# Performance work log

Measured on AMD Instinct MI355X. Metric: run time of the kernel, lower is better.

The kernel has to match this reference:

```python
import jax, jax.numpy as jnp
import numpy as np

N = 1536       # number of agents in the group
T = 20         # track length (only last step used)
H = 64         # hidden_size
E = 16         # embadding_size
M = 128        # PNMLP_hidden_size


def setup_inputs() -> dict:
    key = jax.random.key(0)
    ks = jax.random.split(key, 8)
    s = lambda fan_in: 1.0 / np.sqrt(fan_in)
    return {
        "hidden_state": jax.random.normal(ks[0], (N, H), dtype=jnp.float32),
        "group_track": jax.random.normal(ks[1], (N, T, 2), dtype=jnp.float32),
        "We": jax.random.uniform(ks[2], (2, E), jnp.float32, -s(2), s(2)),
        "be": jax.random.uniform(ks[3], (E,), jnp.float32, -s(2), s(2)),
        "W1": jax.random.uniform(ks[4], (E + H, M), jnp.float32, -s(E + H), s(E + H)),
        "b1": jax.random.uniform(ks[5], (M,), jnp.float32, -s(E + H), s(E + H)),
        "W2": jax.random.uniform(ks[6], (M, H), jnp.float32, -s(M), s(M)),
        "b2": jax.random.uniform(ks[7], (H,), jnp.float32, -s(M), s(M)),
    }


def reference(hidden_state, group_track, We, be, W1, b1, W2, b2):
    # end positions of every track: [N, 2]
    end = group_track[:, -1, :]
    # rel[i, j] = end[j] - end[i]  (neighbor j relative to center i): [N, N, 2]
    rel = end[None, :, :] - end[:, None, :]
    # linear embedding of relative end positions: [N, N, E]
    emb = rel @ We + be
    # concat hidden state (same for all centers) with embedding: [N, N, E+H]
    h = jnp.broadcast_to(hidden_state[None, :, :], (rel.shape[0], rel.shape[1], hidden_state.shape[1]))
    x = jnp.concatenate((h, emb), axis=-1)
    # MLP [E+H -> M -> H] with ReLU after each linear (batch_norm=False)
    x = jax.nn.relu(x @ W1 + b1)
    x = jax.nn.relu(x @ W2 + b2)
    # max-pool over neighbors j for each center i: [N, H]
    return jnp.max(x, axis=1)
```

## Files before the change

kernel.cpp:

```cpp
#include <hip/hip_runtime.h>
#include <hip/hip_fp16.h>


#define NN 1536
#define HH 64
#define EE 16
#define MM 128
#define TT 20
#define NI 2
#define IB 8
#define JSPLIT 8
#define NIGRP (NN / IB)
#define NTILE (96 / JSPLIT)

typedef _Float16 half8 __attribute__((ext_vector_type(8)));
typedef float f32x4 __attribute__((ext_vector_type(4)));

__device__ __forceinline__ void async16(const void* g, void* l) {
  __builtin_amdgcn_global_load_lds(
      (const __attribute__((address_space(1))) unsigned int*)g,
      (__attribute__((address_space(3))) unsigned int*)l, 16, 0, 0);
}

__global__ __launch_bounds__(128) void precompute_kernel(
    const float* __restrict__ hidden, const float* __restrict__ gt,
    const float* __restrict__ We, const float* __restrict__ be,
    const float* __restrict__ W1, const float* __restrict__ b1,
    const float* __restrict__ W2,
    _Float16* __restrict__ Qs, _Float16* __restrict__ P,
    _Float16* __restrict__ W2Ts, float* __restrict__ out)
{
  const int j = blockIdx.x;
  const int m = threadIdx.x;
  const float* hrow = hidden + j * HH;
  float a = 0.f;
  #pragma unroll 8
  for (int h = 0; h < HH; ++h) a = fmaf(hrow[h], W1[h * MM + m], a);
  float ve0 = 0.f, ve1 = 0.f, cm = b1[m];
  #pragma unroll
  for (int e = 0; e < EE; ++e) {
    float w1e = W1[(HH + e) * MM + m];
    ve0 = fmaf(We[e], w1e, ve0);
    ve1 = fmaf(We[EE + e], w1e, ve1);
    cm  = fmaf(be[e], w1e, cm);
  }
  const float e0 = gt[j * (2 * TT) + 2 * (TT - 1)];
  const float e1 = gt[j * (2 * TT) + 2 * (TT - 1) + 1];
  const float p = fmaf(e0, ve0, e1 * ve1);
  P[j * MM + m] = (_Float16)p;
  const int swz = ((((m >> 3) ^ (j & 15)) << 3) | (m & 7));
  Qs[j * MM + swz] = (_Float16)(a + p + cm);
  if (j < HH) W2Ts[j * MM + swz] = (_Float16)W2[m * HH + j];
  if (m < HH) out[j * HH + m] = 0.f;
}

__global__ __launch_bounds__(256) void pairmlp_max_kernel(
    const _Float16* __restrict__ Qs, const _Float16* __restrict__ P,
    const _Float16* __restrict__ W2Ts, const float* __restrict__ b2,
    float* __restrict__ out)
{
  __shared__ __align__(16) _Float16 sW[HH * MM];
  __shared__ __align__(16) _Float16 sQ[2][16 * MM];

  const int tid  = threadIdx.x;
  const int wave = tid >> 6;
  const int lane = tid & 63;
  const int quad = lane >> 4;
  const int lcol = lane & 15;
  const int ig = blockIdx.x % NIGRP;
  const int js = blockIdx.x / NIGRP;
  const int i0 = ig * IB + wave * NI;
  const int jt0 = js * NTILE;

  #pragma unroll
  for (int r = 0; r < 4; ++r)
    async16((const char*)W2Ts + tid * 16 + r * 4096, (char*)sW + tid * 16 + r * 4096);
  async16((const char*)Qs + (size_t)jt0 * 4096 + tid * 16, (char*)sQ[0] + tid * 16);

  half8 pv[NI][4];
  #pragma unroll
  for (int ii = 0; ii < NI; ++ii) {
    const _Float16* prow = P + (i0 + ii) * MM + quad * 8;
    #pragma unroll
    for (int ks = 0; ks < 4; ++ks)
      pv[ii][ks] = *(const half8*)(prow + ks * 32);
  }

  int soff[4];
  #pragma unroll
  for (int ks = 0; ks < 4; ++ks)
    soff[ks] = lcol * MM + ((((ks * 4 + quad) ^ lcol) & 15) << 3);

  float rmax[NI][4];
  #pragma unroll
  for (int ii = 0; ii < NI; ++ii)
    #pragma unroll
    for (int ct = 0; ct < 4; ++ct) rmax[ii][ct] = -1e30f;

  const half8 hz = 0;
  const f32x4 zc = {0.f, 0.f, 0.f, 0.f};

  __syncthreads();

  #pragma unroll 2
  for (int t = 0; t < NTILE; ++t) {
    const int jn = (t + 1 < NTILE) ? (jt0 + t + 1) : jt0;
    async16((const char*)Qs + (size_t)jn * 4096 + tid * 16, (char*)sQ[(t + 1) & 1] + tid * 16);

    const _Float16* qb = sQ[t & 1];
    f32x4 acc[NI][4];
    #pragma unroll
    for (int ks = 0; ks < 4; ++ks) {
      const half8 qg  = *(const half8*)(qb + soff[ks]);
      const half8 bf0 = *(const half8*)(sW + soff[ks]);
      const half8 bf1 = *(const half8*)(sW + soff[ks] + 16 * MM);
      const half8 bf2 = *(const half8*)(sW + soff[ks] + 32 * MM);
      const half8 bf3 = *(const half8*)(sW + soff[ks] + 48 * MM);
      #pragma unroll
      for (int ii = 0; ii < NI; ++ii) {
        half8 s = qg - pv[ii][ks];
        s = __builtin_elementwise_max(s, hz);
        if (ks == 0) {
          acc[ii][0] = __builtin_amdgcn_mfma_f32_16x16x32_f16(s, bf0, zc, 0, 0, 0);
          acc[ii][1] = __builtin_amdgcn_mfma_f32_16x16x32_f16(s, bf1, zc, 0, 0, 0);
          acc[ii][2] = __builtin_amdgcn_mfma_f32_16x16x32_f16(s, bf2, zc, 0, 0, 0);
          acc[ii][3] = __builtin_amdgcn_mfma_f32_16x16x32_f16(s, bf3, zc, 0, 0, 0);
        } else {
          acc[ii][0] = __builtin_amdgcn_mfma_f32_16x16x32_f16(s, bf0, acc[ii][0], 0, 0, 0);
          acc[ii][1] = __builtin_amdgcn_mfma_f32_16x16x32_f16(s, bf1, acc[ii][1], 0, 0, 0);
          acc[ii][2] = __builtin_amdgcn_mfma_f32_16x16x32_f16(s, bf2, acc[ii][2], 0, 0, 0);
          acc[ii][3] = __builtin_amdgcn_mfma_f32_16x16x32_f16(s, bf3, acc[ii][3], 0, 0, 0);
        }
      }
    }

    #pragma unroll
    for (int ii = 0; ii < NI; ++ii)
      #pragma unroll
      for (int ct = 0; ct < 4; ++ct) {
        const float m01 = fmaxf(acc[ii][ct][0], acc[ii][ct][1]);
        const float m23 = fmaxf(acc[ii][ct][2], acc[ii][ct][3]);
        rmax[ii][ct] = fmaxf(rmax[ii][ct], fmaxf(m01, m23));
      }

    __syncthreads();
  }

  #pragma unroll
  for (int ii = 0; ii < NI; ++ii)
    #pragma unroll
    for (int ct = 0; ct < 4; ++ct) {
      float v = rmax[ii][ct];
      v = fmaxf(v, __shfl_xor(v, 16, 64));
      v = fmaxf(v, __shfl_xor(v, 32, 64));
      v = fmaxf(v + b2[ct * 16 + lcol], 0.f);
      if (quad == 0)
        atomicMax((unsigned*)(out + (i0 + ii) * HH + ct * 16 + lcol), __float_as_uint(v));
    }
}

extern "C" void kernel_launch(void* const* d_in, const int* in_sizes, int n_in,
                              void* d_out, int out_size, void* d_ws, size_t ws_size,
                              hipStream_t stream) {
  const float* hidden = (const float*)d_in[0];
  const float* gt     = (const float*)d_in[1];
  const float* We     = (const float*)d_in[2];
  const float* be     = (const float*)d_in[3];
  const float* W1     = (const float*)d_in[4];
  const float* b1     = (const float*)d_in[5];
  const float* W2     = (const float*)d_in[6];
  const float* b2     = (const float*)d_in[7];
  float* out = (float*)d_out;

  _Float16* Qs   = (_Float16*)d_ws;
  _Float16* Ph   = Qs + NN * MM;
  _Float16* W2Ts = Ph + NN * MM;

  precompute_kernel<<<NN, 128, 0, stream>>>(hidden, gt, We, be, W1, b1, W2, Qs, Ph, W2Ts, out);
  pairmlp_max_kernel<<<NIGRP * JSPLIT, 256, 0, stream>>>(Qs, Ph, W2Ts, b2, out);
}
```

Before: 114.4 us.

## Hold W2 MFMA fragments in registers instead of LDS and halve j-split

Each wave now loads its W2 B-operand fragments (16 half8 values) straight from global memory into registers once, so the 16 KB shared-memory copy of W2 and the four LDS reads per k-step go away. W2T is stored unswizzled for this. The j-split drops from 8 to 4, so each block handles twice as many neighbor tiles and issues fewer atomics per output. The cost is 64 extra VGPRs per thread and fewer blocks, which means less parallelism across the GPU.

```diff
diff --git a/kernel.cpp b/kernel.cpp
--- a/kernel.cpp
+++ b/kernel.cpp
@@ -9,7 +9,7 @@
 #define TT 20
 #define NI 2
 #define IB 8
-#define JSPLIT 8
+#define JSPLIT 4
 #define NIGRP (NN / IB)
 #define NTILE (96 / JSPLIT)
 
@@ -28,7 +28,7 @@
     const float* __restrict__ W1, const float* __restrict__ b1,
     const float* __restrict__ W2,
     _Float16* __restrict__ Qs, _Float16* __restrict__ P,
-    _Float16* __restrict__ W2Ts, float* __restrict__ out)
+    _Float16* __restrict__ W2T, float* __restrict__ out)
 {
   const int j = blockIdx.x;
   const int m = threadIdx.x;
@@ -50,16 +50,15 @@
   P[j * MM + m] = (_Float16)p;
   const int swz = ((((m >> 3) ^ (j & 15)) << 3) | (m & 7));
   Qs[j * MM + swz] = (_Float16)(a + p + cm);
-  if (j < HH) W2Ts[j * MM + swz] = (_Float16)W2[m * HH + j];
+  if (j < HH) W2T[j * MM + m] = (_Float16)W2[m * HH + j];
   if (m < HH) out[j * HH + m] = 0.f;
 }
 
 __global__ __launch_bounds__(256) void pairmlp_max_kernel(
     const _Float16* __restrict__ Qs, const _Float16* __restrict__ P,
-    const _Float16* __restrict__ W2Ts, const float* __restrict__ b2,
+    const _Float16* __restrict__ W2T, const float* __restrict__ b2,
     float* __restrict__ out)
 {
-  __shared__ __align__(16) _Float16 sW[HH * MM];
   __shared__ __align__(16) _Float16 sQ[2][16 * MM];
 
   const int tid  = threadIdx.x;
@@ -72,10 +71,16 @@
   const int i0 = ig * IB + wave * NI;
   const int jt0 = js * NTILE;
 
+  async16((const char*)Qs + (size_t)jt0 * 4096 + tid * 16, (char*)sQ[0] + tid * 16);
+
+  half8 bfrag[4][4];
   #pragma unroll
-  for (int r = 0; r < 4; ++r)
-    async16((const char*)W2Ts + tid * 16 + r * 4096, (char*)sW + tid * 16 + r * 4096);
-  async16((const char*)Qs + (size_t)jt0 * 4096 + tid * 16, (char*)sQ[0] + tid * 16);
+  for (int ct = 0; ct < 4; ++ct) {
+    const _Float16* wrow = W2T + (ct * 16 + lcol) * MM + quad * 8;
+    #pragma unroll
+    for (int ks = 0; ks < 4; ++ks)
+      bfrag[ct][ks] = *(const half8*)(wrow + ks * 32);
+  }
 
   half8 pv[NI][4];
   #pragma unroll
@@ -111,25 +116,19 @@
     f32x4 acc[NI][4];
     #pragma unroll
     for (int ks = 0; ks < 4; ++ks) {
-      const half8 qg  = *(const half8*)(qb + soff[ks]);
-      const half8 bf0 = *(const half8*)(sW + soff[ks]);
-      const half8 bf1 = *(const half8*)(sW + soff[ks] + 16 * MM);
-      const half8 bf2 = *(const half8*)(sW + soff[ks] + 32 * MM);
-      const half8 bf3 = *(const half8*)(sW + soff[ks] + 48 * MM);
+      const half8 qg = *(const half8*)(qb + soff[ks]);
       #pragma unroll
       for (int ii = 0; ii < NI; ++ii) {
         half8 s = qg - pv[ii][ks];
         s = __builtin_elementwise_max(s, hz);
         if (ks == 0) {
-          acc[ii][0] = __builtin_amdgcn_mfma_f32_16x16x32_f16(s, bf0, zc, 0, 0, 0);
-          acc[ii][1] = __builtin_amdgcn_mfma_f32_16x16x32_f16(s, bf1, zc, 0, 0, 0);
-          acc[ii][2] = __builtin_amdgcn_mfma_f32_16x16x32_f16(s, bf2, zc, 0, 0, 0);
-          acc[ii][3] = __builtin_amdgcn_mfma_f32_16x16x32_f16(s, bf3, zc, 0, 0, 0);
+          #pragma unroll
+          for (int ct = 0; ct < 4; ++ct)
+            acc[ii][ct] = __builtin_amdgcn_mfma_f32_16x16x32_f16(s, bfrag[ct][0], zc, 0, 0, 0);
         } else {
-          acc[ii][0] = __builtin_amdgcn_mfma_f32_16x16x32_f16(s, bf0, acc[ii][0], 0, 0, 0);
-          acc[ii][1] = __builtin_amdgcn_mfma_f32_16x16x32_f16(s, bf1, acc[ii][1], 0, 0, 0);
-          acc[ii][2] = __builtin_amdgcn_mfma_f32_16x16x32_f16(s, bf2, acc[ii][2], 0, 0, 0);
-          acc[ii][3] = __builtin_amdgcn_mfma_f32_16x16x32_f16(s, bf3, acc[ii][3], 0, 0, 0);
+          #pragma unroll
+          for (int ct = 0; ct < 4; ++ct)
+            acc[ii][ct] = __builtin_amdgcn_mfma_f32_16x16x32_f16(s, bfrag[ct][ks], acc[ii][ct], 0, 0, 0);
         }
       }
     }
@@ -172,10 +171,10 @@
   const float* b2     = (const float*)d_in[7];
   float* out = (float*)d_out;
 
-  _Float16* Qs   = (_Float16*)d_ws;
-  _Float16* Ph   = Qs + NN * MM;
-  _Float16* W2Ts = Ph + NN * MM;
+  _Float16* Qs  = (_Float16*)d_ws;
+  _Float16* Ph  = Qs + NN * MM;
+  _Float16* W2T = Ph + NN * MM;
 
-  precompute_kernel<<<NN, 128, 0, stream>>>(hidden, gt, We, be, W1, b1, W2, Qs, Ph, W2Ts, out);
-  pairmlp_max_kernel<<<NIGRP * JSPLIT, 256, 0, stream>>>(Qs, Ph, W2Ts, b2, out);
+  precompute_kernel<<<NN, 128, 0, stream>>>(hidden, gt, We, be, W1, b1, W2, Qs, Ph, W2T, out);
+  pairmlp_max_kernel<<<NIGRP * JSPLIT, 256, 0, stream>>>(Qs, Ph, W2T, b2, out);
 }
```

Result: slower. 118.1 us (+3.2%).
